# Performance work log

Measured on AMD Instinct MI355X. Metric: run time of the kernel, lower is better.

The kernel has to match this reference:

```python
import jax, jax.numpy as jnp
import numpy as np

B, T, D, HD = 8, 2048, 768, 64

def setup_inputs() -> dict:
    key = jax.random.key(0)
    k1, k2, k3, k4 = jax.random.split(key, 4)
    scale = 1.0 / np.sqrt(D)
    return {
        "x": jax.random.normal(k1, (B, T, D), dtype=jnp.float32),
        "Wq": jax.random.normal(k2, (D, HD), dtype=jnp.float32) * scale,
        "Wk": jax.random.normal(k3, (D, HD), dtype=jnp.float32) * scale,
        "Wv": jax.random.normal(k4, (D, HD), dtype=jnp.float32) * scale,
    }

def reference(x, Wq, Wk, Wv):
    # q,k,v: [B,T,HD]
    q = jnp.einsum('btd,dh->bth', x, Wq)
    k = jnp.einsum('btd,dh->bth', x, Wk)
    v = jnp.einsum('btd,dh->bth', x, Wv)
    dk = q.shape[-1]
    # scores: [B,T,T], scaled then causally masked with -inf
    scores = jnp.einsum('bqh,bkh->bqk', q, k) / jnp.sqrt(jnp.float32(dk))
    Tq = scores.shape[-1]
    causal = jnp.tril(jnp.ones((Tq, Tq), dtype=bool))
    scores = jnp.where(causal, scores, -jnp.inf)
    attn = jax.nn.softmax(scores, axis=-1)  # dropout rate 0 (eval mode)
    return jnp.einsum('bqk,bkh->bqh', attn, v)
```

## Files before the change

### kernel.cpp

```cpp
#include <hip/hip_runtime.h>
#include <hip/hip_bf16.h>
#include <stdint.h>

#define B_  8
#define T_  2048
#define D_  768
#define HD_ 64
#define M_  (B_ * T_)

typedef short s16x8 __attribute__((ext_vector_type(8)));
typedef float f32x4 __attribute__((ext_vector_type(4)));
typedef unsigned int u32;

union Frag { uint4 u; s16x8 h; };

__device__ __forceinline__ unsigned short f2bf(float f) {
    unsigned u = __builtin_bit_cast(unsigned, f);
    u += 0x7FFFu + ((u >> 16) & 1u);
    return (unsigned short)(u >> 16);
}
__device__ __forceinline__ unsigned pack_bf16x2(float lo, float hi) {
    return (unsigned)f2bf(lo) | ((unsigned)f2bf(hi) << 16);
}
__device__ __forceinline__ unsigned cvt_pk(float lo, float hi) {
    unsigned r;
    asm("v_cvt_pk_bf16_f32 %0, %1, %2" : "=v"(r) : "v"(lo), "v"(hi));
    return r;
}

__device__ __forceinline__ void gl_lds16(const void* g, void* l) {
    __builtin_amdgcn_global_load_lds(
        (const __attribute__((address_space(1))) u32*)g,
        (__attribute__((address_space(3))) u32*)l, 16, 0, 0);
}

__global__ __launch_bounds__(64) void prep_pk(const float* __restrict__ Wq,
                                              const float* __restrict__ Wk,
                                              const float* __restrict__ Wv,
                                              unsigned short* __restrict__ pk) {
    int nb = blockIdx.x / 24, kk = blockIdx.x % 24;
    int lane = threadIdx.x, g = lane >> 4, t = lane & 15;
    int mat = nb >> 2, col = (nb & 3) * 16 + t;
    const float* W = (mat == 0) ? Wq : (mat == 1) ? Wk : Wv;
    float s = (mat == 0) ? 0.18033688011112042f : 1.0f;
    float v[8];
#pragma unroll
    for (int e = 0; e < 8; e++)
        v[e] = W[(size_t)(kk * 32 + g * 8 + e) * HD_ + col] * s;
    uint4 u;
    u.x = pack_bf16x2(v[0], v[1]);
    u.y = pack_bf16x2(v[2], v[3]);
    u.z = pack_bf16x2(v[4], v[5]);
    u.w = pack_bf16x2(v[6], v[7]);
    *(uint4*)(pk + ((size_t)blockIdx.x * 64 + lane) * 8) = u;
}

__global__ __launch_bounds__(256, 2) void qkv_proj(const float* __restrict__ x,
                                                   const unsigned short* __restrict__ pk,
                                                   unsigned short* __restrict__ qo,
                                                   unsigned short* __restrict__ ko,
                                                   unsigned short* __restrict__ vt) {
    __shared__ char xs[4][8192];

    int tid = threadIdx.x, w = tid >> 6, lane = tid & 63;
    int g = lane >> 4, t = lane & 15;
    int m0 = blockIdx.x * 32;

    auto STAGE = [&](int jb) {
        int buf = jb & 3;
#pragma unroll
        for (int h = 0; h < 2; h++) {
            int s = tid + h * 256;
            int row = s >> 4;
            int a = (s & 15) ^ (row & 15);
            gl_lds16(x + (size_t)(m0 + row) * D_ + jb * 64 + a * 4,
                     &xs[buf][(w * 64 + h * 256) * 16]);
        }
    };

    const unsigned short* wp = pk + (size_t)w * 36864;
    auto LOADB = [&](Frag (&bb)[6], int jb) {
#pragma unroll
        for (int j = 0; j < 3; j++)
#pragma unroll
            for (int c = 0; c < 2; c++)
                bb[j * 2 + c].u = *(const uint4*)(wp + ((size_t)(j * 24 + jb * 2 + c) * 64 + lane) * 8);
    };

    f32x4 acc[3][2];
#pragma unroll
    for (int j = 0; j < 3; j++)
#pragma unroll
        for (int mf = 0; mf < 2; mf++) acc[j][mf] = (f32x4){0.f, 0.f, 0.f, 0.f};

    Frag bA[6], bB[6];
    LOADB(bA, 0);
    STAGE(0); STAGE(1); STAGE(2);

    auto PHASE = [&](int jb, Frag (&bb)[6]) {
        asm volatile("s_waitcnt vmcnt(8)" ::: "memory");
        __builtin_amdgcn_s_barrier();
        int buf = jb & 3;
        Frag af[2][2];
#pragma unroll
        for (int mf = 0; mf < 2; mf++) {
            int r32 = mf * 16 + t;
#pragma unroll
            for (int c = 0; c < 2; c++) {
                float4 f0 = *(const float4*)(&xs[buf][r32 * 256 + (((c * 8 + g * 2 + 0) ^ t) * 16)]);
                float4 f1 = *(const float4*)(&xs[buf][r32 * 256 + (((c * 8 + g * 2 + 1) ^ t) * 16)]);
                af[mf][c].u.x = cvt_pk(f0.x, f0.y);
                af[mf][c].u.y = cvt_pk(f0.z, f0.w);
                af[mf][c].u.z = cvt_pk(f1.x, f1.y);
                af[mf][c].u.w = cvt_pk(f1.z, f1.w);
            }
        }
        __builtin_amdgcn_s_setprio(1);
#pragma unroll
        for (int j = 0; j < 3; j++)
#pragma unroll
            for (int c = 0; c < 2; c++) {
                acc[j][0] = __builtin_amdgcn_mfma_f32_16x16x32_bf16(af[0][c].h, bb[j * 2 + c].h, acc[j][0], 0, 0, 0);
                acc[j][1] = __builtin_amdgcn_mfma_f32_16x16x32_bf16(af[1][c].h, bb[j * 2 + c].h, acc[j][1], 0, 0, 0);
            }
        __builtin_amdgcn_s_setprio(0);
        __builtin_amdgcn_s_barrier();
        if (jb + 3 < 12) STAGE(jb + 3);
    };

#pragma unroll 1
    for (int jb2 = 0; jb2 < 12; jb2 += 2) {
        if (jb2 + 1 < 12) LOADB(bB, jb2 + 1);
        PHASE(jb2, bA);
        if (jb2 + 2 < 12) LOADB(bA, jb2 + 2);
        PHASE(jb2 + 1, bB);
    }

#pragma unroll
    for (int j = 0; j < 3; j++) {
        int nb = w * 3 + j;
        int col = (nb & 3) * 16 + t;
#pragma unroll
        for (int mf = 0; mf < 2; mf++) {
            int row0 = m0 + mf * 16;
            if (nb < 8) {
                unsigned short* dst = (nb < 4) ? qo : ko;
#pragma unroll
                for (int r = 0; r < 4; r++)
                    dst[(size_t)(row0 + g * 4 + r) * HD_ + col] = f2bf(acc[j][mf][r]);
            } else {
                int bb = m0 >> 11;
                int trow = (row0 & 2047) + g * 4;
                uint2 pkk;
                pkk.x = cvt_pk(acc[j][mf][0], acc[j][mf][1]);
                pkk.y = cvt_pk(acc[j][mf][2], acc[j][mf][3]);
                *(uint2*)(vt + (((size_t)(bb * HD_ + col)) << 11) + trow) = pkk;
            }
        }
    }
}

__global__ __launch_bounds__(512) void attn(const unsigned short* __restrict__ qw,
                                            const unsigned short* __restrict__ kw,
                                            const unsigned short* __restrict__ vt,
                                            float* __restrict__ out) {
    __shared__ char smem[65536];

    int tid = threadIdx.x, wv = tid >> 6, lane = tid & 63;
    int g = lane >> 4, t = lane & 15;
    int qw_ = wv & 1, ks = wv >> 1;
    int blk = blockIdx.x;
    int b = blk & 7, idx = blk >> 3;
    int qblk = (idx < 32) ? idx : 95 - idx;
    int q0 = qblk * 32;
    int qrow = q0 + qw_ * 16 + t;
    size_t bbase = (size_t)b * T_;
    int nt = qblk + 1;
    int nq = (nt + 3) >> 2;

    const unsigned short* kp = kw + bbase * HD_;
    const unsigned short* vp = vt + ((size_t)(b * HD_) << 11);

    Frag qf[2];
#pragma unroll
    for (int c = 0; c < 2; c++)
        qf[c].u = *(const uint4*)(qw + (bbase + qrow) * HD_ + c * 32 + g * 8);

    auto STAGE = [&](int j) {
        int jj = (j < nt) ? j : (nt - 1);
        int kv0 = jj * 32;
        if (wv < 4) {
            int s = wv * 64 + lane;
            int row = s >> 3, a = (s & 7) ^ (row & 7);
            gl_lds16(kp + (size_t)(kv0 + row) * HD_ + a * 8,
                     smem + (j & 7) * 4096 + wv * 1024);
        } else {
            int s = (wv - 4) * 64 + lane;
            int d = s >> 2, a = (s & 3) ^ (d & 3) ^ ((d >> 2) & 3);
            gl_lds16(vp + ((size_t)d << 11) + kv0 + a * 8,
                     smem + 32768 + (j & 7) * 4096 + (wv - 4) * 1024);
        }
    };

    f32x4 o[4];
#pragma unroll
    for (int d = 0; d < 4; d++) o[d] = (f32x4){0.f, 0.f, 0.f, 0.f};
    float lacc = 0.0f;

#pragma unroll
    for (int j0 = 0; j0 < 8; j0++) STAGE(j0);

#pragma unroll 1
    for (int i = 0; i < nq; i++) {
        asm volatile("s_waitcnt vmcnt(4)" ::: "memory");
        __builtin_amdgcn_s_barrier();
        int j = 4 * i + ks;
        if (j < nt) {
            const char* KB = smem + (j & 7) * 4096;
            const char* VB = smem + 32768 + (j & 7) * 4096;
            int kv0 = j * 32;
            f32x4 st[2];
            st[0] = (f32x4){0.f, 0.f, 0.f, 0.f};
            st[1] = (f32x4){0.f, 0.f, 0.f, 0.f};
            __builtin_amdgcn_s_setprio(1);
#pragma unroll
            for (int kf = 0; kf < 2; kf++) {
                int row = kf * 16 + t, m7 = row & 7;
#pragma unroll
                for (int c = 0; c < 2; c++) {
                    Frag ka;
                    ka.u = *(const uint4*)(KB + row * 128 + (((c * 4 + g) ^ m7) * 16));
                    st[kf] = __builtin_amdgcn_mfma_f32_16x16x32_bf16(ka.h, qf[c].h, st[kf], 0, 0, 0);
                }
            }
            __builtin_amdgcn_s_setprio(0);

            if (j == qblk) {
#pragma unroll
                for (int kf = 0; kf < 2; kf++)
#pragma unroll
                    for (int r = 0; r < 4; r++)
                        if (kv0 + kf * 16 + g * 4 + r > qrow) st[kf][r] = -1e30f;
            }

            float p0[4], p1[4];
#pragma unroll
            for (int r = 0; r < 4; r++) {
                p0[r] = exp2f(st[0][r]);
                p1[r] = exp2f(st[1][r]);
            }
            lacc += (p0[0] + p0[1]) + (p0[2] + p0[3]) + (p1[0] + p1[1]) + (p1[2] + p1[3]);

            unsigned pk0[2], pk1[2];
            pk0[0] = cvt_pk(p0[0], p0[1]); pk0[1] = cvt_pk(p0[2], p0[3]);
            pk1[0] = cvt_pk(p1[0], p1[1]); pk1[1] = cvt_pk(p1[2], p1[3]);
            Frag pf;
            unsigned pw[4];
#pragma unroll
            for (int w2 = 0; w2 < 4; w2++) {
                int src = ((g & 1) * 2 + (w2 >> 1)) * 16 + t;
                unsigned vlo = (unsigned)__shfl((int)pk0[w2 & 1], src, 64);
                unsigned vhi = (unsigned)__shfl((int)pk1[w2 & 1], src, 64);
                pw[w2] = (lane < 32) ? vlo : vhi;
            }
            pf.u.x = pw[0]; pf.u.y = pw[1]; pf.u.z = pw[2]; pf.u.w = pw[3];

            __builtin_amdgcn_s_setprio(1);
#pragma unroll
            for (int df = 0; df < 4; df++) {
                int row = df * 16 + t;
                int sw = g ^ (row & 3) ^ ((row >> 2) & 3);
                Frag va;
                va.u = *(const uint4*)(VB + row * 64 + sw * 16);
                o[df] = __builtin_amdgcn_mfma_f32_16x16x32_bf16(va.h, pf.h, o[df], 0, 0, 0);
            }
            __builtin_amdgcn_s_setprio(0);
        }
        __builtin_amdgcn_s_barrier();
#pragma unroll
        for (int u = 0; u < 4; u++) STAGE(4 * i + 8 + u);
    }

    asm volatile("s_waitcnt vmcnt(0)" ::: "memory");
    __syncthreads();

    lacc += __shfl_xor(lacc, 16);
    lacc += __shfl_xor(lacc, 32);
    float* MO = (float*)smem;
    if (ks) {
        int base = ((qw_ * 3 + (ks - 1)) * 64 + lane) * 17;
#pragma unroll
        for (int df = 0; df < 4; df++)
#pragma unroll
            for (int r = 0; r < 4; r++) MO[base + df * 4 + r] = o[df][r];
        MO[base + 16] = lacc;
    }
    __syncthreads();
    if (ks == 0) {
        float ls = lacc;
#pragma unroll
        for (int kk = 0; kk < 3; kk++)
            ls += MO[((qw_ * 3 + kk) * 64 + lane) * 17 + 16];
        float inv = 1.0f / ls;
        float* op = out + (bbase + qrow) * HD_;
#pragma unroll
        for (int df = 0; df < 4; df++)
#pragma unroll
            for (int r = 0; r < 4; r++) {
                float s = o[df][r];
#pragma unroll
                for (int kk = 0; kk < 3; kk++)
                    s += MO[((qw_ * 3 + kk) * 64 + lane) * 17 + df * 4 + r];
                op[df * 16 + g * 4 + r] = s * inv;
            }
    }
}

extern "C" void kernel_launch(void* const* d_in, const int* in_sizes, int n_in,
                              void* d_out, int out_size, void* d_ws, size_t ws_size,
                              hipStream_t stream) {
    const float* x  = (const float*)d_in[0];
    const float* Wq = (const float*)d_in[1];
    const float* Wk = (const float*)d_in[2];
    const float* Wv = (const float*)d_in[3];
    char* ws = (char*)d_ws;
    unsigned short* pkw = (unsigned short*)ws;
    unsigned short* qw = (unsigned short*)(ws + 294912);
    unsigned short* kw = (unsigned short*)(ws + 294912 + 2097152);
    unsigned short* vt = (unsigned short*)(ws + 294912 + 4194304);
    float* out = (float*)d_out;

    hipLaunchKernelGGL(prep_pk, dim3(288), dim3(64), 0, stream, Wq, Wk, Wv, pkw);
    hipLaunchKernelGGL(qkv_proj, dim3(M_ / 32), dim3(256), 0, stream, x, pkw, qw, kw, vt);
    hipLaunchKernelGGL(attn, dim3(512), dim3(512), 0, stream, qw, kw, vt, out);
}
```

Measured before the change: 47.22 us.

## Switch attention to 32x32 MFMA with 4-wave blocks; triple-buffer projection weights

The attention kernel now uses 256-thread blocks where each wave covers all 32 query rows of a block with 32x32x16 bf16 MFMAs. This replaces the 16x16 tiles split across two query waves, and it simplifies the P-fragment shuffle to xor-32 exchanges. Block ordering is reversed so that the heaviest causal blocks launch first. The projection kernel now triple-buffers the weight fragments with explicit vmcnt waits and a fully unrolled loop. These changes aim to reduce MFMA issue count and shuffle overhead, at the cost of fewer waves per block and higher register pressure.

Result: slower. 49.21 us (+4.2%).

```diff
diff --git a/kernel.cpp b/kernel.cpp
--- a/kernel.cpp
+++ b/kernel.cpp
@@ -10,6 +10,7 @@
 
 typedef short s16x8 __attribute__((ext_vector_type(8)));
 typedef float f32x4 __attribute__((ext_vector_type(4)));
+typedef float f32x16 __attribute__((ext_vector_type(16)));
 typedef unsigned int u32;
 
 union Frag { uint4 u; s16x8 h; };
@@ -93,14 +94,21 @@
 #pragma unroll
         for (int mf = 0; mf < 2; mf++) acc[j][mf] = (f32x4){0.f, 0.f, 0.f, 0.f};
 
-    Frag bA[6], bB[6];
-    LOADB(bA, 0);
+    Frag bfr[3][6];
+    LOADB(bfr[0], 0);
+    LOADB(bfr[1], 1);
     STAGE(0); STAGE(1); STAGE(2);
 
-    auto PHASE = [&](int jb, Frag (&bb)[6]) {
-        asm volatile("s_waitcnt vmcnt(8)" ::: "memory");
+#pragma unroll
+    for (int jb = 0; jb < 12; jb++) {
+        if (jb + 2 < 12) LOADB(bfr[(jb + 2) % 3], jb + 2);
+        if (jb == 0)       asm volatile("s_waitcnt vmcnt(10)" ::: "memory");
+        else if (jb == 10) asm volatile("s_waitcnt vmcnt(8)"  ::: "memory");
+        else if (jb == 11) asm volatile("s_waitcnt vmcnt(0)"  ::: "memory");
+        else               asm volatile("s_waitcnt vmcnt(16)" ::: "memory");
         __builtin_amdgcn_s_barrier();
         int buf = jb & 3;
+
         Frag af[2][2];
 #pragma unroll
         for (int mf = 0; mf < 2; mf++) {
@@ -120,20 +128,12 @@
         for (int j = 0; j < 3; j++)
 #pragma unroll
             for (int c = 0; c < 2; c++) {
-                acc[j][0] = __builtin_amdgcn_mfma_f32_16x16x32_bf16(af[0][c].h, bb[j * 2 + c].h, acc[j][0], 0, 0, 0);
-                acc[j][1] = __builtin_amdgcn_mfma_f32_16x16x32_bf16(af[1][c].h, bb[j * 2 + c].h, acc[j][1], 0, 0, 0);
+                acc[j][0] = __builtin_amdgcn_mfma_f32_16x16x32_bf16(af[0][c].h, bfr[jb % 3][j * 2 + c].h, acc[j][0], 0, 0, 0);
+                acc[j][1] = __builtin_amdgcn_mfma_f32_16x16x32_bf16(af[1][c].h, bfr[jb % 3][j * 2 + c].h, acc[j][1], 0, 0, 0);
             }
         __builtin_amdgcn_s_setprio(0);
         __builtin_amdgcn_s_barrier();
         if (jb + 3 < 12) STAGE(jb + 3);
-    };
-
-#pragma unroll 1
-    for (int jb2 = 0; jb2 < 12; jb2 += 2) {
-        if (jb2 + 1 < 12) LOADB(bB, jb2 + 1);
-        PHASE(jb2, bA);
-        if (jb2 + 2 < 12) LOADB(bA, jb2 + 2);
-        PHASE(jb2 + 1, bB);
     }
 
 #pragma unroll
@@ -160,20 +160,19 @@
     }
 }
 
-__global__ __launch_bounds__(512) void attn(const unsigned short* __restrict__ qw,
+__global__ __launch_bounds__(256) void attn(const unsigned short* __restrict__ qw,
                                             const unsigned short* __restrict__ kw,
                                             const unsigned short* __restrict__ vt,
                                             float* __restrict__ out) {
     __shared__ char smem[65536];
 
     int tid = threadIdx.x, wv = tid >> 6, lane = tid & 63;
-    int g = lane >> 4, t = lane & 15;
-    int qw_ = wv & 1, ks = wv >> 1;
+    int hi = lane >> 5, l31 = lane & 31;
     int blk = blockIdx.x;
     int b = blk & 7, idx = blk >> 3;
-    int qblk = (idx < 32) ? idx : 95 - idx;
+    int qblk = (idx < 32) ? (63 - idx) : (idx - 32);
     int q0 = qblk * 32;
-    int qrow = q0 + qw_ * 16 + t;
+    int qg = q0 + l31;
     size_t bbase = (size_t)b * T_;
     int nt = qblk + 1;
     int nq = (nt + 3) >> 2;
@@ -181,98 +180,100 @@
     const unsigned short* kp = kw + bbase * HD_;
     const unsigned short* vp = vt + ((size_t)(b * HD_) << 11);
 
-    Frag qf[2];
-#pragma unroll
-    for (int c = 0; c < 2; c++)
-        qf[c].u = *(const uint4*)(qw + (bbase + qrow) * HD_ + c * 32 + g * 8);
+    Frag qf[4];
+#pragma unroll
+    for (int c = 0; c < 4; c++)
+        qf[c].u = *(const uint4*)(qw + (bbase + qg) * HD_ + c * 16 + hi * 8);
 
     auto STAGE = [&](int j) {
         int jj = (j < nt) ? j : (nt - 1);
-        int kv0 = jj * 32;
-        if (wv < 4) {
-            int s = wv * 64 + lane;
-            int row = s >> 3, a = (s & 7) ^ (row & 7);
-            gl_lds16(kp + (size_t)(kv0 + row) * HD_ + a * 8,
-                     smem + (j & 7) * 4096 + wv * 1024);
-        } else {
-            int s = (wv - 4) * 64 + lane;
-            int d = s >> 2, a = (s & 3) ^ (d & 3) ^ ((d >> 2) & 3);
-            gl_lds16(vp + ((size_t)d << 11) + kv0 + a * 8,
-                     smem + 32768 + (j & 7) * 4096 + (wv - 4) * 1024);
-        }
+        int kv0 = jj * 32, buf = j & 7;
+        int kr = wv * 8 + (lane >> 3);
+        int ka = (lane & 7) ^ (kr & 7);
+        gl_lds16(kp + (size_t)(kv0 + kr) * HD_ + ka * 8, smem + buf * 4096 + wv * 1024);
+        int vd = wv * 16 + (lane >> 2);
+        int va = (lane & 3) ^ (vd & 3) ^ ((vd >> 2) & 3);
+        gl_lds16(vp + ((size_t)vd << 11) + kv0 + va * 8, smem + 32768 + buf * 4096 + wv * 1024);
     };
 
-    f32x4 o[4];
-#pragma unroll
-    for (int d = 0; d < 4; d++) o[d] = (f32x4){0.f, 0.f, 0.f, 0.f};
-    float lacc = 0.0f;
+    f32x16 o0, o1;
+#pragma unroll
+    for (int r = 0; r < 16; r++) { o0[r] = 0.f; o1[r] = 0.f; }
+    float lacc = 0.f;
 
 #pragma unroll
     for (int j0 = 0; j0 < 8; j0++) STAGE(j0);
 
 #pragma unroll 1
     for (int i = 0; i < nq; i++) {
-        asm volatile("s_waitcnt vmcnt(4)" ::: "memory");
+        asm volatile("s_waitcnt vmcnt(8)" ::: "memory");
         __builtin_amdgcn_s_barrier();
-        int j = 4 * i + ks;
+        int j = 4 * i + wv;
         if (j < nt) {
             const char* KB = smem + (j & 7) * 4096;
             const char* VB = smem + 32768 + (j & 7) * 4096;
             int kv0 = j * 32;
-            f32x4 st[2];
-            st[0] = (f32x4){0.f, 0.f, 0.f, 0.f};
-            st[1] = (f32x4){0.f, 0.f, 0.f, 0.f};
+            f32x16 st;
+#pragma unroll
+            for (int r = 0; r < 16; r++) st[r] = 0.f;
             __builtin_amdgcn_s_setprio(1);
 #pragma unroll
-            for (int kf = 0; kf < 2; kf++) {
-                int row = kf * 16 + t, m7 = row & 7;
-#pragma unroll
-                for (int c = 0; c < 2; c++) {
-                    Frag ka;
-                    ka.u = *(const uint4*)(KB + row * 128 + (((c * 4 + g) ^ m7) * 16));
-                    st[kf] = __builtin_amdgcn_mfma_f32_16x16x32_bf16(ka.h, qf[c].h, st[kf], 0, 0, 0);
+            for (int c = 0; c < 4; c++) {
+                Frag ka;
+                ka.u = *(const uint4*)(KB + l31 * 128 + (((c * 2 + hi) ^ (l31 & 7)) * 16));
+                st = __builtin_amdgcn_mfma_f32_32x32x16_bf16(ka.h, qf[c].h, st, 0, 0, 0);
+            }
+            __builtin_amdgcn_s_setprio(0);
+
+            if (j == qblk) {
+#pragma unroll
+                for (int r = 0; r < 16; r++) {
+                    int key = kv0 + (r & 3) + 8 * (r >> 2) + 4 * hi;
+                    if (key > qg) st[r] = -1e30f;
                 }
             }
-            __builtin_amdgcn_s_setprio(0);
-
-            if (j == qblk) {
-#pragma unroll
-                for (int kf = 0; kf < 2; kf++)
-#pragma unroll
-                    for (int r = 0; r < 4; r++)
-                        if (kv0 + kf * 16 + g * 4 + r > qrow) st[kf][r] = -1e30f;
-            }
-
-            float p0[4], p1[4];
-#pragma unroll
-            for (int r = 0; r < 4; r++) {
-                p0[r] = exp2f(st[0][r]);
-                p1[r] = exp2f(st[1][r]);
-            }
-            lacc += (p0[0] + p0[1]) + (p0[2] + p0[3]) + (p1[0] + p1[1]) + (p1[2] + p1[3]);
-
-            unsigned pk0[2], pk1[2];
-            pk0[0] = cvt_pk(p0[0], p0[1]); pk0[1] = cvt_pk(p0[2], p0[3]);
-            pk1[0] = cvt_pk(p1[0], p1[1]); pk1[1] = cvt_pk(p1[2], p1[3]);
-            Frag pf;
-            unsigned pw[4];
-#pragma unroll
-            for (int w2 = 0; w2 < 4; w2++) {
-                int src = ((g & 1) * 2 + (w2 >> 1)) * 16 + t;
-                unsigned vlo = (unsigned)__shfl((int)pk0[w2 & 1], src, 64);
-                unsigned vhi = (unsigned)__shfl((int)pk1[w2 & 1], src, 64);
-                pw[w2] = (lane < 32) ? vlo : vhi;
-            }
-            pf.u.x = pw[0]; pf.u.y = pw[1]; pf.u.z = pw[2]; pf.u.w = pw[3];
+
+            float p[16], ss = 0.f;
+#pragma unroll
+            for (int r = 0; r < 16; r++) { p[r] = exp2f(st[r]); ss += p[r]; }
+            lacc += ss;
+
+            u32 A0 = cvt_pk(p[0], p[1]),   A1 = cvt_pk(p[2], p[3]);
+            u32 B0 = cvt_pk(p[4], p[5]),   B1 = cvt_pk(p[6], p[7]);
+            u32 C0 = cvt_pk(p[8], p[9]),   C1 = cvt_pk(p[10], p[11]);
+            u32 D0 = cvt_pk(p[12], p[13]), D1 = cvt_pk(p[14], p[15]);
+            u32 A0x = (u32)__shfl_xor((int)A0, 32);
+            u32 A1x = (u32)__shfl_xor((int)A1, 32);
+            u32 B0x = (u32)__shfl_xor((int)B0, 32);
+            u32 B1x = (u32)__shfl_xor((int)B1, 32);
+            u32 C0x = (u32)__shfl_xor((int)C0, 32);
+            u32 C1x = (u32)__shfl_xor((int)C1, 32);
+            u32 D0x = (u32)__shfl_xor((int)D0, 32);
+            u32 D1x = (u32)__shfl_xor((int)D1, 32);
+            Frag pf0, pf1;
+            pf0.u.x = hi ? B0x : A0;
+            pf0.u.y = hi ? B1x : A1;
+            pf0.u.z = hi ? B0  : A0x;
+            pf0.u.w = hi ? B1  : A1x;
+            pf1.u.x = hi ? D0x : C0;
+            pf1.u.y = hi ? D1x : C1;
+            pf1.u.z = hi ? D0  : C0x;
+            pf1.u.w = hi ? D1  : C1x;
 
             __builtin_amdgcn_s_setprio(1);
-#pragma unroll
-            for (int df = 0; df < 4; df++) {
-                int row = df * 16 + t;
-                int sw = g ^ (row & 3) ^ ((row >> 2) & 3);
+            {
+                int sw0 = (l31 & 3) ^ ((l31 >> 2) & 3);
                 Frag va;
-                va.u = *(const uint4*)(VB + row * 64 + sw * 16);
-                o[df] = __builtin_amdgcn_mfma_f32_16x16x32_bf16(va.h, pf.h, o[df], 0, 0, 0);
+                va.u = *(const uint4*)(VB + l31 * 64 + (((hi) ^ sw0) * 16));
+                o0 = __builtin_amdgcn_mfma_f32_32x32x16_bf16(va.h, pf0.h, o0, 0, 0, 0);
+                va.u = *(const uint4*)(VB + l31 * 64 + (((2 + hi) ^ sw0) * 16));
+                o0 = __builtin_amdgcn_mfma_f32_32x32x16_bf16(va.h, pf1.h, o0, 0, 0, 0);
+                int d1 = 32 + l31;
+                int sw1 = (d1 & 3) ^ ((d1 >> 2) & 3);
+                va.u = *(const uint4*)(VB + d1 * 64 + (((hi) ^ sw1) * 16));
+                o1 = __builtin_amdgcn_mfma_f32_32x32x16_bf16(va.h, pf0.h, o1, 0, 0, 0);
+                va.u = *(const uint4*)(VB + d1 * 64 + (((2 + hi) ^ sw1) * 16));
+                o1 = __builtin_amdgcn_mfma_f32_32x32x16_bf16(va.h, pf1.h, o1, 0, 0, 0);
             }
             __builtin_amdgcn_s_setprio(0);
         }
@@ -284,35 +285,33 @@
     asm volatile("s_waitcnt vmcnt(0)" ::: "memory");
     __syncthreads();
 
-    lacc += __shfl_xor(lacc, 16);
     lacc += __shfl_xor(lacc, 32);
     float* MO = (float*)smem;
-    if (ks) {
-        int base = ((qw_ * 3 + (ks - 1)) * 64 + lane) * 17;
-#pragma unroll
-        for (int df = 0; df < 4; df++)
-#pragma unroll
-            for (int r = 0; r < 4; r++) MO[base + df * 4 + r] = o[df][r];
-        MO[base + 16] = lacc;
+    if (wv) {
+        int base = ((wv - 1) * 64 + lane) * 33;
+#pragma unroll
+        for (int r = 0; r < 16; r++) { MO[base + r] = o0[r]; MO[base + 16 + r] = o1[r]; }
+        MO[base + 32] = lacc;
     }
     __syncthreads();
-    if (ks == 0) {
+    if (wv == 0) {
         float ls = lacc;
 #pragma unroll
-        for (int kk = 0; kk < 3; kk++)
-            ls += MO[((qw_ * 3 + kk) * 64 + lane) * 17 + 16];
+        for (int k = 0; k < 3; k++) ls += MO[(k * 64 + lane) * 33 + 32];
         float inv = 1.0f / ls;
-        float* op = out + (bbase + qrow) * HD_;
-#pragma unroll
-        for (int df = 0; df < 4; df++)
-#pragma unroll
-            for (int r = 0; r < 4; r++) {
-                float s = o[df][r];
-#pragma unroll
-                for (int kk = 0; kk < 3; kk++)
-                    s += MO[((qw_ * 3 + kk) * 64 + lane) * 17 + df * 4 + r];
-                op[df * 16 + g * 4 + r] = s * inv;
-            }
+        float* op = out + (bbase + qg) * HD_;
+#pragma unroll
+        for (int r = 0; r < 16; r++) {
+            float s0 = o0[r], s1 = o1[r];
+#pragma unroll
+            for (int k = 0; k < 3; k++) {
+                s0 += MO[(k * 64 + lane) * 33 + r];
+                s1 += MO[(k * 64 + lane) * 33 + 16 + r];
+            }
+            int dr = (r & 3) + 8 * (r >> 2) + 4 * hi;
+            op[dr] = s0 * inv;
+            op[32 + dr] = s1 * inv;
+        }
     }
 }
 
@@ -332,5 +331,5 @@
 
     hipLaunchKernelGGL(prep_pk, dim3(288), dim3(64), 0, stream, Wq, Wk, Wv, pkw);
     hipLaunchKernelGGL(qkv_proj, dim3(M_ / 32), dim3(256), 0, stream, x, pkw, qw, kw, vt);
-    hipLaunchKernelGGL(attn, dim3(512), dim3(512), 0, stream, qw, kw, vt, out);
-}
+    hipLaunchKernelGGL(attn, dim3(512), dim3(256), 0, stream, qw, kw, vt, out);
+}
```
